# Kernel tuning notes

Measured on AMD Instinct MI355X. Metric: run time of the kernel, lower is better.

The kernel has to match this reference:

```python
import jax, jax.numpy as jnp
import numpy as np

BLOCK = 8
WIN = 3
PAD = WIN - 1


def _dct_mat(b, dtype):
    # Orthonormal DCT-II matrix: D[k, n] = s_k * sqrt(2/b) * cos(pi*(2n+1)k/(2b))
    n = np.arange(b)
    k = n[:, None]
    D = np.sqrt(2.0 / b) * np.cos(np.pi * (2 * n[None, :] + 1) * k / (2 * b))
    D[0, :] *= 1.0 / np.sqrt(2.0)
    return jnp.asarray(D, dtype=dtype)


def setup_inputs() -> dict:
    key = jax.random.key(0)
    k1, k2 = jax.random.split(key)
    x = jax.random.normal(k1, (8, 64, 256, 256), dtype=jnp.float32)
    conv_w = jax.random.normal(k2, (64, 64, WIN), dtype=jnp.float32) * 0.05
    conv_b = jnp.zeros((64,), dtype=jnp.float32)
    return {"x": x, "conv_w": conv_w, "conv_b": conv_b}


def reference(x, conv_w, conv_b):
    b = BLOCK
    bsz, ch, H, W = x.shape
    nH, nW = H // b, W // b
    n = nH * nW
    D = _dct_mat(b, x.dtype)

    # blockify: (bsz, ch, n_blocks, b, b)
    blk = x.reshape(bsz, ch, nH, b, nW, b).transpose(0, 1, 2, 4, 3, 5)
    blk = blk.reshape(bsz, ch, n, b, b)

    # block 2D DCT: D @ X @ D^T
    coef = jnp.einsum('kn,bcxnm,lm->bcxkl', D, blk, D)
    coef = coef.reshape(bsz, ch, n, b * b)

    # FreqConv: causal-right-padded Conv1d over the b*b frequency axis
    y = coef.transpose(0, 2, 1, 3).reshape(bsz * n, ch, b * b)
    y = jnp.pad(y, ((0, 0), (0, 0), (0, PAD)))
    y = jax.lax.conv_general_dilated(
        y, conv_w, window_strides=(1,), padding=[(0, 0)],
        dimension_numbers=('NCH', 'OIH', 'NCH'), feature_group_count=1)
    y = y + conv_b[None, :, None]
    out_ch = y.shape[1]
    y = y.reshape(bsz, n, out_ch, b * b).transpose(0, 2, 1, 3)

    # block 2D IDCT: D^T @ X @ D
    y = y.reshape(bsz, out_ch, n, b, b)
    img = jnp.einsum('kn,bcxkl,lm->bcxnm', D, y, D)

    # deblockify back to (bsz, out_ch, H, W)
    img = img.reshape(bsz, out_ch, nH, nW, b, b).transpose(0, 1, 2, 4, 3, 5)
    return img.reshape(bsz, out_ch, H, W)
```

## Files before the change

kernel.cpp:

```cpp
#include <hip/hip_runtime.h>


#define THREADS 256
#define HW 256
#define CH 64
#define W_STRIDE 200
#define CT_ROW 72
#define CT_SAMPLE (66 * CT_ROW)
#define WB_USHORTS (64 * W_STRIDE)

typedef __attribute__((ext_vector_type(8))) short short8b;
typedef __attribute__((ext_vector_type(4))) float f32x4;
typedef __attribute__((ext_vector_type(4))) unsigned short us4;

__device__ inline unsigned short f2bf(float f) {
    unsigned u = __builtin_bit_cast(unsigned, f);
    u += 0x7FFFu + ((u >> 16) & 1u);
    return (unsigned short)(u >> 16);
}
__device__ inline float bf2f(unsigned short h) {
    unsigned u = ((unsigned)h) << 16;
    return __builtin_bit_cast(float, u);
}

__device__ __constant__ static const float D8[8][8] = {
  { 0.3535533906f, 0.3535533906f, 0.3535533906f, 0.3535533906f, 0.3535533906f, 0.3535533906f, 0.3535533906f, 0.3535533906f },
  { 0.4903926402f, 0.4157348062f, 0.2777851165f, 0.0975451610f,-0.0975451610f,-0.2777851165f,-0.4157348062f,-0.4903926402f },
  { 0.4619397663f, 0.1913417162f,-0.1913417162f,-0.4619397663f,-0.4619397663f,-0.1913417162f, 0.1913417162f, 0.4619397663f },
  { 0.4157348062f,-0.0975451610f,-0.4903926402f,-0.2777851165f, 0.2777851165f, 0.4903926402f, 0.0975451610f,-0.4157348062f },
  { 0.3535533906f,-0.3535533906f,-0.3535533906f, 0.3535533906f, 0.3535533906f,-0.3535533906f,-0.3535533906f, 0.3535533906f },
  { 0.2777851165f,-0.4903926402f, 0.0975451610f, 0.4157348062f,-0.4157348062f,-0.0975451610f, 0.4903926402f,-0.2777851165f },
  { 0.1913417162f,-0.4619397663f, 0.4619397663f,-0.1913417162f,-0.1913417162f, 0.4619397663f,-0.4619397663f, 0.1913417162f },
  { 0.0975451610f,-0.2777851165f, 0.4157348062f,-0.4903926402f, 0.4903926402f,-0.4157348062f, 0.2777851165f,-0.0975451610f },
};

__global__ __launch_bounds__(THREADS, 2)
void dct_freq_conv_kernel(const float* __restrict__ x,
                          const float* __restrict__ conv_w,
                          const float* __restrict__ conv_b,
                          float* __restrict__ out)
{
    extern __shared__ char smem[];
    unsigned short* Wb    = (unsigned short*)smem;
    unsigned short* Ct    = (unsigned short*)(smem + 2 * WB_USHORTS);
    float*          biasL = (float*)(smem + 2 * WB_USHORTS + 2 * 4 * CT_SAMPLE);

    const int tid = threadIdx.x;
    const int bz  = blockIdx.z;
    const int by  = blockIdx.y;
    const int bx0 = blockIdx.x * 4;

    const int c   = tid >> 2;
    const int blk = tid & 3;

    #pragma unroll 4
    for (int j = tid; j < 64 * 192; j += THREADS) {
        int o = j / 192;
        int r = j - o * 192;
        int i = r / 3;
        int w = r - i * 3;
        Wb[o * W_STRIDE + w * 64 + i] = f2bf(conv_w[j]);
    }
    if (tid < 64) biasL[tid] = conv_b[tid];
    {
        int s = tid >> 6, i = tid & 63;
        Ct[s * CT_SAMPLE + 64 * CT_ROW + i] = 0;
        Ct[s * CT_SAMPLE + 65 * CT_ROW + i] = 0;
    }

    {
        const float* xp = x + ((((size_t)bz * CH + c) * HW + by * 8) * HW
                               + (bx0 + blk) * 8);
        float v[8][8];
        #pragma unroll
        for (int r = 0; r < 8; ++r) {
            float4 a = *reinterpret_cast<const float4*>(xp + r * HW);
            float4 b = *reinterpret_cast<const float4*>(xp + r * HW + 4);
            v[r][0] = a.x; v[r][1] = a.y; v[r][2] = a.z; v[r][3] = a.w;
            v[r][4] = b.x; v[r][5] = b.y; v[r][6] = b.z; v[r][7] = b.w;
        }
        #pragma unroll
        for (int n = 0; n < 8; ++n) {
            float r[8];
            #pragma unroll
            for (int l = 0; l < 8; ++l) {
                float s = 0.f;
                #pragma unroll
                for (int m = 0; m < 8; ++m) s = fmaf(v[n][m], D8[l][m], s);
                r[l] = s;
            }
            #pragma unroll
            for (int l = 0; l < 8; ++l) v[n][l] = r[l];
        }
        unsigned short* ctw = Ct + blk * CT_SAMPLE + c;
        #pragma unroll
        for (int l = 0; l < 8; ++l) {
            #pragma unroll
            for (int k = 0; k < 8; ++k) {
                float s = 0.f;
                #pragma unroll
                for (int n = 0; n < 8; ++n) s = fmaf(D8[k][n], v[n][l], s);
                ctw[(k * 8 + l) * CT_ROW] = f2bf(s);
            }
        }
    }

    __syncthreads();

    const int wid  = tid >> 6;
    const int lane = tid & 63;
    const int lr   = lane & 15;
    const int lq   = lane >> 4;

    f32x4 acc[4][4];
    #pragma unroll
    for (int m = 0; m < 4; ++m)
        #pragma unroll
        for (int n = 0; n < 4; ++n)
            acc[m][n] = (f32x4){0.f, 0.f, 0.f, 0.f};

    unsigned short* CtP = Ct + wid * CT_SAMPLE;

    #pragma unroll
    for (int kc = 0; kc < 6; ++kc) {
        const int w  = kc >> 1;
        const int i0 = (kc & 1) * 32 + 8 * lq;
        short8b a[4], b[4];
        #pragma unroll
        for (int m = 0; m < 4; ++m)
            a[m] = *(const short8b*)&Wb[(m * 16 + lr) * W_STRIDE + w * 64 + i0];
        #pragma unroll
        for (int n = 0; n < 4; ++n)
            b[n] = *(const short8b*)&CtP[(n * 16 + lr + w) * CT_ROW + i0];
        #pragma unroll
        for (int m = 0; m < 4; ++m)
            #pragma unroll
            for (int n = 0; n < 4; ++n)
                acc[m][n] = __builtin_amdgcn_mfma_f32_16x16x32_bf16(
                    a[m], b[n], acc[m][n], 0, 0, 0);
    }

    #pragma unroll
    for (int mt = 0; mt < 4; ++mt) {
        const int o0 = mt * 16 + lq * 4;
        #pragma unroll
        for (int nt = 0; nt < 4; ++nt) {
            const int t = nt * 16 + lr;
            us4 pk;
            #pragma unroll
            for (int j = 0; j < 4; ++j)
                pk[j] = f2bf(acc[mt][nt][j] + biasL[o0 + j]);
            *(us4*)&CtP[t * CT_ROW + o0] = pk;
        }
    }

    __syncthreads();

    {
        const unsigned short* yb = Ct + blk * CT_SAMPLE + c;
        float y[64];
        #pragma unroll
        for (int t = 0; t < 64; ++t) y[t] = bf2f(yb[t * CT_ROW]);

        #pragma unroll
        for (int l = 0; l < 8; ++l) {
            float r[8];
            #pragma unroll
            for (int n = 0; n < 8; ++n) {
                float s = 0.f;
                #pragma unroll
                for (int k = 0; k < 8; ++k) s = fmaf(D8[k][n], y[k * 8 + l], s);
                r[n] = s;
            }
            #pragma unroll
            for (int n = 0; n < 8; ++n) y[n * 8 + l] = r[n];
        }
        float* op = out + ((((size_t)bz * CH + c) * HW + by * 8) * HW
                           + (bx0 + blk) * 8);
        #pragma unroll
        for (int n = 0; n < 8; ++n) {
            float o8[8];
            #pragma unroll
            for (int m = 0; m < 8; ++m) {
                float s = 0.f;
                #pragma unroll
                for (int l = 0; l < 8; ++l) s = fmaf(y[n * 8 + l], D8[l][m], s);
                o8[m] = s;
            }
            *reinterpret_cast<float4*>(op + n * HW)     = make_float4(o8[0], o8[1], o8[2], o8[3]);
            *reinterpret_cast<float4*>(op + n * HW + 4) = make_float4(o8[4], o8[5], o8[6], o8[7]);
        }
    }
}

extern "C" void kernel_launch(void* const* d_in, const int* in_sizes, int n_in,
                              void* d_out, int out_size, void* d_ws, size_t ws_size,
                              hipStream_t stream) {
    const float* x  = (const float*)d_in[0];
    const float* cw = (const float*)d_in[1];
    const float* cb = (const float*)d_in[2];
    float* o        = (float*)d_out;

    const size_t lds_bytes = 2 * WB_USHORTS + 2 * 4 * CT_SAMPLE + 64 * sizeof(float);
    hipFuncSetAttribute(reinterpret_cast<const void*>(dct_freq_conv_kernel),
                        hipFuncAttributeMaxDynamicSharedMemorySize,
                        (int)lds_bytes);

    dim3 grid(8, 32, 8);
    dct_freq_conv_kernel<<<grid, dim3(THREADS), lds_bytes, stream>>>(x, cw, cb, o);
}
```

Baseline: 258.8 us.

## Pre-convert conv weights in a prep kernel and stream them from global memory

A small kernel now converts and transposes the conv weights to bf16 once per launch, writing them to workspace. The main kernel reads MFMA weight fragments straight from global/L2 instead of staging the whole weight matrix in LDS. This removes the per-block weight staging loop and cuts LDS use, which allows raising launch bounds to 4 blocks per CU. The GEMM operands are also swapped so the output lands transposed in LDS, letting the inverse-DCT stage read 8 contiguous values per vector load, and the bias add moves into that stage. The cost is repeated global loads of the weights inside the MFMA loop, plus an extra kernel launch.

```diff
diff --git a/kernel.cpp b/kernel.cpp
--- a/kernel.cpp
+++ b/kernel.cpp
@@ -4,14 +4,14 @@
 #define THREADS 256
 #define HW 256
 #define CH 64
-#define W_STRIDE 200
 #define CT_ROW 72
 #define CT_SAMPLE (66 * CT_ROW)
-#define WB_USHORTS (64 * W_STRIDE)
+#define LDS_BYTES (4 * CT_SAMPLE * 2)
 
 typedef __attribute__((ext_vector_type(8))) short short8b;
 typedef __attribute__((ext_vector_type(4))) float f32x4;
 typedef __attribute__((ext_vector_type(4))) unsigned short us4;
+typedef __attribute__((ext_vector_type(8))) unsigned short us8;
 
 __device__ inline unsigned short f2bf(float f) {
     unsigned u = __builtin_bit_cast(unsigned, f);
@@ -34,16 +34,24 @@
   { 0.0975451610f,-0.2777851165f, 0.4157348062f,-0.4903926402f, 0.4903926402f,-0.4157348062f, 0.2777851165f,-0.0975451610f },
 };
 
-__global__ __launch_bounds__(THREADS, 2)
+__global__ __launch_bounds__(256)
+void wt_prep_kernel(const float* __restrict__ conv_w, unsigned short* __restrict__ wt) {
+    int j = blockIdx.x * 256 + threadIdx.x;
+    int w = j >> 12;
+    int rem = j & 4095;
+    int o = rem >> 6;
+    int i = rem & 63;
+    wt[j] = f2bf(conv_w[o * 192 + i * 3 + w]);
+}
+
+__global__ __launch_bounds__(THREADS, 4)
 void dct_freq_conv_kernel(const float* __restrict__ x,
-                          const float* __restrict__ conv_w,
+                          const unsigned short* __restrict__ wt,
                           const float* __restrict__ conv_b,
                           float* __restrict__ out)
 {
     extern __shared__ char smem[];
-    unsigned short* Wb    = (unsigned short*)smem;
-    unsigned short* Ct    = (unsigned short*)(smem + 2 * WB_USHORTS);
-    float*          biasL = (float*)(smem + 2 * WB_USHORTS + 2 * 4 * CT_SAMPLE);
+    unsigned short* Ct = (unsigned short*)smem;
 
     const int tid = threadIdx.x;
     const int bz  = blockIdx.z;
@@ -53,15 +61,6 @@
     const int c   = tid >> 2;
     const int blk = tid & 3;
 
-    #pragma unroll 4
-    for (int j = tid; j < 64 * 192; j += THREADS) {
-        int o = j / 192;
-        int r = j - o * 192;
-        int i = r / 3;
-        int w = r - i * 3;
-        Wb[o * W_STRIDE + w * 64 + i] = f2bf(conv_w[j]);
-    }
-    if (tid < 64) biasL[tid] = conv_b[tid];
     {
         int s = tid >> 6, i = tid & 63;
         Ct[s * CT_SAMPLE + 64 * CT_ROW + i] = 0;
@@ -114,10 +113,10 @@
 
     f32x4 acc[4][4];
     #pragma unroll
-    for (int m = 0; m < 4; ++m)
-        #pragma unroll
-        for (int n = 0; n < 4; ++n)
-            acc[m][n] = (f32x4){0.f, 0.f, 0.f, 0.f};
+    for (int n = 0; n < 4; ++n)
+        #pragma unroll
+        for (int m = 0; m < 4; ++m)
+            acc[n][m] = (f32x4){0.f, 0.f, 0.f, 0.f};
 
     unsigned short* CtP = Ct + wid * CT_SAMPLE;
 
@@ -127,41 +126,44 @@
         const int i0 = (kc & 1) * 32 + 8 * lq;
         short8b a[4], b[4];
         #pragma unroll
+        for (int n = 0; n < 4; ++n)
+            a[n] = *(const short8b*)&CtP[(n * 16 + lr + w) * CT_ROW + i0];
+        #pragma unroll
         for (int m = 0; m < 4; ++m)
-            a[m] = *(const short8b*)&Wb[(m * 16 + lr) * W_STRIDE + w * 64 + i0];
+            b[m] = *(const short8b*)&wt[(w * 64 + m * 16 + lr) * 64 + i0];
         #pragma unroll
         for (int n = 0; n < 4; ++n)
-            b[n] = *(const short8b*)&CtP[(n * 16 + lr + w) * CT_ROW + i0];
-        #pragma unroll
-        for (int m = 0; m < 4; ++m)
-            #pragma unroll
-            for (int n = 0; n < 4; ++n)
-                acc[m][n] = __builtin_amdgcn_mfma_f32_16x16x32_bf16(
-                    a[m], b[n], acc[m][n], 0, 0, 0);
+            #pragma unroll
+            for (int m = 0; m < 4; ++m)
+                acc[n][m] = __builtin_amdgcn_mfma_f32_16x16x32_bf16(
+                    a[n], b[m], acc[n][m], 0, 0, 0);
     }
 
     #pragma unroll
-    for (int mt = 0; mt < 4; ++mt) {
-        const int o0 = mt * 16 + lq * 4;
-        #pragma unroll
-        for (int nt = 0; nt < 4; ++nt) {
-            const int t = nt * 16 + lr;
+    for (int n = 0; n < 4; ++n) {
+        const int t0 = n * 16 + 4 * lq;
+        #pragma unroll
+        for (int m = 0; m < 4; ++m) {
+            const int o = m * 16 + lr;
             us4 pk;
             #pragma unroll
-            for (int j = 0; j < 4; ++j)
-                pk[j] = f2bf(acc[mt][nt][j] + biasL[o0 + j]);
-            *(us4*)&CtP[t * CT_ROW + o0] = pk;
+            for (int j = 0; j < 4; ++j) pk[j] = f2bf(acc[n][m][j]);
+            *(us4*)&CtP[o * CT_ROW + t0] = pk;
         }
     }
 
     __syncthreads();
 
     {
-        const unsigned short* yb = Ct + blk * CT_SAMPLE + c;
+        const unsigned short* yb = Ct + blk * CT_SAMPLE + c * CT_ROW;
+        const float bias = conv_b[c];
         float y[64];
         #pragma unroll
-        for (int t = 0; t < 64; ++t) y[t] = bf2f(yb[t * CT_ROW]);
-
+        for (int j = 0; j < 8; ++j) {
+            us8 v = *(const us8*)&yb[j * 8];
+            #pragma unroll
+            for (int e = 0; e < 8; ++e) y[j * 8 + e] = bf2f(v[e]) + bias;
+        }
         #pragma unroll
         for (int l = 0; l < 8; ++l) {
             float r[8];
@@ -200,12 +202,13 @@
     const float* cw = (const float*)d_in[1];
     const float* cb = (const float*)d_in[2];
     float* o        = (float*)d_out;
-
-    const size_t lds_bytes = 2 * WB_USHORTS + 2 * 4 * CT_SAMPLE + 64 * sizeof(float);
+    unsigned short* wtb = (unsigned short*)d_ws;
+
+    wt_prep_kernel<<<dim3(48), dim3(256), 0, stream>>>(cw, wtb);
+
     hipFuncSetAttribute(reinterpret_cast<const void*>(dct_freq_conv_kernel),
                         hipFuncAttributeMaxDynamicSharedMemorySize,
-                        (int)lds_bytes);
-
+                        (int)LDS_BYTES);
     dim3 grid(8, 32, 8);
-    dct_freq_conv_kernel<<<grid, dim3(THREADS), lds_bytes, stream>>>(x, cw, cb, o);
-}
+    dct_freq_conv_kernel<<<grid, dim3(THREADS), LDS_BYTES, stream>>>(x, wtb, cb, o);
+}
```

New measurement: 266.2 us. 2.8% more time.
